# Performance work log

Hardware: AMD Instinct MI355X
Metric: run time of the kernel (lower is better)

Reference implementation:

```python
import jax, jax.numpy as jnp
import numpy as np

D_MODEL = 1024
HEADS = 16
D_K = D_MODEL // HEADS
D_FF = 4096
B, S = 4, 2048
EPS = 1e-5


def _layer_norm(x, gamma, beta):
    mu = jnp.mean(x, axis=-1, keepdims=True)
    var = jnp.mean(jnp.square(x - mu), axis=-1, keepdims=True)
    return (x - mu) * jax.lax.rsqrt(var + EPS) * gamma + beta


def setup_inputs() -> dict:
    key = jax.random.key(0)
    ks = jax.random.split(key, 16)
    s_in = 1.0 / np.sqrt(D_MODEL)
    s_ff = 1.0 / np.sqrt(D_FF)
    inp = {
        "x": jax.random.normal(ks[0], (B, S, D_MODEL), dtype=jnp.float32),
        "src_mask": jnp.ones((B, 1, 1, S), dtype=jnp.int32),
        "Wq": jax.random.uniform(ks[1], (D_MODEL, D_MODEL), jnp.float32, -s_in, s_in),
        "bq": jnp.zeros((D_MODEL,), jnp.float32),
        "Wk": jax.random.uniform(ks[2], (D_MODEL, D_MODEL), jnp.float32, -s_in, s_in),
        "bk": jnp.zeros((D_MODEL,), jnp.float32),
        "Wv": jax.random.uniform(ks[3], (D_MODEL, D_MODEL), jnp.float32, -s_in, s_in),
        "bv": jnp.zeros((D_MODEL,), jnp.float32),
        "Wo": jax.random.uniform(ks[4], (D_MODEL, D_MODEL), jnp.float32, -s_in, s_in),
        "bo": jnp.zeros((D_MODEL,), jnp.float32),
        "W1": jax.random.uniform(ks[5], (D_MODEL, D_FF), jnp.float32, -s_in, s_in),
        "b1": jnp.zeros((D_FF,), jnp.float32),
        "W2": jax.random.uniform(ks[6], (D_FF, D_MODEL), jnp.float32, -s_ff, s_ff),
        "b2": jnp.zeros((D_MODEL,), jnp.float32),
        "g1": jnp.ones((D_MODEL,), jnp.float32),
        "be1": jnp.zeros((D_MODEL,), jnp.float32),
        "g2": jnp.ones((D_MODEL,), jnp.float32),
        "be2": jnp.zeros((D_MODEL,), jnp.float32),
    }
    return inp


def reference(x, src_mask, Wq, bq, Wk, bk, Wv, bv, Wo, bo, W1, b1, W2, b2, g1, be1, g2, be2):
    Bn, L, _ = x.shape
    # Self-attention (dropout=0 / eval)
    q = (x @ Wq + bq).reshape(Bn, L, HEADS, D_K).transpose(0, 2, 1, 3)  # [B,H,L,dk]
    k = (x @ Wk + bk).reshape(Bn, L, HEADS, D_K).transpose(0, 2, 1, 3)
    v = (x @ Wv + bv).reshape(Bn, L, HEADS, D_K).transpose(0, 2, 1, 3)
    scores = jnp.einsum("bhqd,bhkd->bhqk", q, k) / np.sqrt(D_K).astype(np.float32)
    scores = jnp.where(src_mask == 0, -jnp.inf, scores)
    attn = jax.nn.softmax(scores, axis=-1)
    out = jnp.einsum("bhqk,bhkd->bhqd", attn, v)
    out = out.transpose(0, 2, 1, 3).reshape(Bn, L, D_MODEL)
    attn_out = out @ Wo + bo
    x = _layer_norm(x + attn_out, g1, be1)
    # FFN
    ffn = jax.nn.relu(x @ W1 + b1) @ W2 + b2
    x = _layer_norm(x + ffn, g2, be2)
    return x
```

## Files before the change

kernel.cpp:

```cpp
#include <hip/hip_runtime.h>
#include <hip/hip_bf16.h>
#include <cstdint>
#include <cstddef>

typedef __bf16 bf16;
typedef __bf16 bf16x8 __attribute__((ext_vector_type(8)));
typedef float  f32x4  __attribute__((ext_vector_type(4)));
typedef unsigned short u16x4 __attribute__((ext_vector_type(4)));
typedef uint32_t u32x4 __attribute__((ext_vector_type(4)));

static constexpr int D_MODEL = 1024;
static constexpr int HEADS   = 16;
static constexpr int D_KH    = 64;
static constexpr int D_FF    = 4096;
static constexpr int BATCH   = 4;
static constexpr int SEQ     = 2048;
static constexpr int MROWS   = BATCH * SEQ;
static constexpr float QSCALE = 0.18033688011f;

#define VMCNT(n) asm volatile("s_waitcnt vmcnt(" #n ")" ::: "memory")
#define LGKM0()                                            \
  do {                                                     \
    asm volatile("s_waitcnt lgkmcnt(0)" ::: "memory");     \
    __builtin_amdgcn_sched_barrier(0);                     \
  } while (0)

__device__ __forceinline__ unsigned short bfbits(float f) {
  return __builtin_bit_cast(unsigned short, (bf16)f);
}
__device__ __forceinline__ float bf2f(unsigned short u) {
  return __builtin_bit_cast(float, (uint32_t)u << 16);
}

__device__ __forceinline__ void gload_lds16(const void* g, void* l) {
  __builtin_amdgcn_global_load_lds(
      (__attribute__((address_space(1))) uint32_t*)(uintptr_t)g,
      (__attribute__((address_space(3))) uint32_t*)(uintptr_t)l, 16, 0, 0);
}

struct PrepArgs {
  const float* x; bf16* xb;
  const int* mask; uint32_t* flags;
  const float* w1; const float* w2; const float* wx[4];
  bf16* w1t; bf16* w2t; bf16* wxt[4];
};
__global__ void k_prep(PrepArgs p) {
  __shared__ float tile[64][65];
  const int t = blockIdx.x;
  if (t < 4096) {
    int i = (t * 256 + threadIdx.x) * 8;
    const float4* q = (const float4*)(p.x + i);
    float4 a = q[0], b = q[1];
    bf16x8 v;
    v[0] = (bf16)a.x; v[1] = (bf16)a.y; v[2] = (bf16)a.z; v[3] = (bf16)a.w;
    v[4] = (bf16)b.x; v[5] = (bf16)b.y; v[6] = (bf16)b.z; v[7] = (bf16)b.w;
    *(bf16x8*)(p.xb + i) = v;
    return;
  }
  if (t == 4096) {
    __shared__ uint32_t sb[4];
    int tid = threadIdx.x;
    if (tid < 4) sb[tid] = 0;
    __syncthreads();
    if (tid < 128) {
      int b = tid >> 5, tt = tid & 31;
      const int4* q = (const int4*)(p.mask + b * SEQ + tt * 64);
      int all = 1;
#pragma unroll
      for (int i = 0; i < 16; ++i) {
        int4 v = q[i];
        all &= v.x & v.y & v.z & v.w;
      }
      if (all) atomicOr(&sb[b], 1u << tt);
    }
    __syncthreads();
    if (tid < 4) p.flags[tid] = sb[tid];
    return;
  }
  int u = t - 4097;
  const float* W;
  bf16* Wt;
  int K, N, k0, n0;
  if (u < 1024) {
    W = p.w1; Wt = p.w1t; K = 1024; N = 4096;
    k0 = (u & 15) * 64; n0 = (u >> 4) * 64;
  } else if (u < 2048) {
    int v = u - 1024;
    W = p.w2; Wt = p.w2t; K = 4096; N = 1024;
    k0 = (v & 63) * 64; n0 = (v >> 6) * 64;
  } else {
    int v = u - 2048;
    int which = v >> 8, vv = v & 255;
    W = p.wx[which]; Wt = p.wxt[which]; K = 1024; N = 1024;
    k0 = (vv & 15) * 64; n0 = (vv >> 4) * 64;
  }
  int c = threadIdx.x & 63, r0 = threadIdx.x >> 6;
#pragma unroll
  for (int i = 0; i < 16; ++i) {
    int r = r0 + i * 4;
    tile[r][c] = W[(size_t)(k0 + r) * N + n0 + c];
  }
  __syncthreads();
#pragma unroll
  for (int i = 0; i < 16; ++i) {
    int r = r0 + i * 4;
    Wt[(size_t)(n0 + r) * K + k0 + c] = (bf16)tile[c][r];
  }
}

enum { EP_RELU = 0, EP_O16 = 1, EP_QKV = 2 };

template <int EPI, int NREP>
__global__ __launch_bounds__(512, 2) void k_gemm8(
    const bf16* __restrict__ A, const bf16* __restrict__ Bt,
    const float* __restrict__ bias, const float* __restrict__ bias2,
    const float* __restrict__ bias3,
    void* __restrict__ Cout, void* __restrict__ C2, void* __restrict__ C3,
    int N, int K) {
  extern __shared__ char smem[];
  constexpr int BN = NREP * 64;
  constexpr int HB = NREP / 2;
  const int tid = threadIdx.x;
  const int lane = tid & 63;
  const int wid = tid >> 6;
  const int wm = wid >> 2, wn = wid & 3;
  const int l15 = lane & 15, l4 = lane >> 4;
  const int bx = blockIdx.x, by = blockIdx.y;
  const int NI = K >> 7;

  const int c0 = tid, c1 = tid + 512;
  const bf16* baseA0 = A + (size_t)(bx * 256 + (c0 >> 3)) * K + ((c0 & 7) ^ ((c0 >> 3) & 7)) * 8;
  const bf16* baseA1 = A + (size_t)(bx * 256 + (c1 >> 3)) * K + ((c1 & 7) ^ ((c1 >> 3) & 7)) * 8;
  const bf16* baseB0 = Bt + (size_t)(by * BN + (c0 >> 3)) * K + ((c0 & 7) ^ ((c0 >> 3) & 7)) * 8;
  const bf16* baseB1 = Bt + (size_t)(by * BN + (c1 >> 3)) * K + ((c1 & 7) ^ ((c1 >> 3) & 7)) * 8;
  const size_t rowK128 = (size_t)128 * K;

  auto stA = [&](int h, int t, int buf) {
    gload_lds16(baseA0 + h * rowK128 + t * 64, smem + buf * 32768 + h * 16384 + c0 * 16);
    gload_lds16(baseA1 + h * rowK128 + t * 64, smem + buf * 32768 + h * 16384 + c1 * 16);
  };
  auto stB = [&](int h, int t, int buf) {
    gload_lds16(baseB0 + h * rowK128 + t * 64,
                smem + 65536 + buf * (HB * 16384) + h * 16384 + c0 * 16);
    gload_lds16(baseB1 + h * rowK128 + t * 64,
                smem + 65536 + buf * (HB * 16384) + h * 16384 + c1 * 16);
  };

  const int ch0 = (l4 ^ (l15 & 7)) * 16;
  const int ch1 = ((4 + l4) ^ (l15 & 7)) * 16;
  const int aoff = l15 * 128;
  int boffh[NREP];
#pragma unroll
  for (int n = 0; n < NREP; ++n) {
    int rB = wn * (NREP * 16) + n * 16 + l15;
    boffh[n] = (rB >> 7) * 16384 + (rB & 127) * 128;
  }

  f32x4 acc[8][NREP] = {};
  bf16x8 breg[NREP][2];

  stA(0, 0, 0); stA(1, 0, 0); stB(0, 0, 0);
  if constexpr (HB == 2) stB(1, 0, 0);
  stA(0, 1, 1); stA(1, 1, 1); stB(0, 1, 1);
  if constexpr (HB == 2) stB(1, 1, 1);

  for (int i = 0; i < NI; ++i) {
    const int t1 = 2 * i + 1, t2 = 2 * i + 2;
    const bool notfirst = (i > 0), notlast = (i + 1 < NI);
#pragma unroll
    for (int p = 0; p < 8; ++p) {
      const int q = p & 3;
      const char* Ab = smem + (p >> 2) * 32768 + wm * 16384;
      const char* Bb = smem + 65536 + (p >> 2) * (HB * 16384);
      if (p == 0) {
        if (notfirst) {
          stA(0, t1, 1);
          VMCNT(2);
        } else {
          if constexpr (HB == 2) VMCNT(8); else VMCNT(6);
        }
        __builtin_amdgcn_s_barrier();
      } else if (p == 4) {
        if (notlast) {
          stA(0, t2, 0);
          VMCNT(2);
        } else {
          VMCNT(0);
        }
        __builtin_amdgcn_s_barrier();
      }
      if (q == 0) {
#pragma unroll
        for (int n = 0; n < NREP; ++n) {
          breg[n][0] = *(const bf16x8*)(Bb + boffh[n] + ch0);
          breg[n][1] = *(const bf16x8*)(Bb + boffh[n] + ch1);
        }
      }
      bf16x8 a0k0 = *(const bf16x8*)(Ab + (2 * q + 0) * 2048 + aoff + ch0);
      bf16x8 a0k1 = *(const bf16x8*)(Ab + (2 * q + 0) * 2048 + aoff + ch1);
      bf16x8 a1k0 = *(const bf16x8*)(Ab + (2 * q + 1) * 2048 + aoff + ch0);
      bf16x8 a1k1 = *(const bf16x8*)(Ab + (2 * q + 1) * 2048 + aoff + ch1);
      if (p == 1) { if (notfirst) stA(1, t1, 1); }
      else if (p == 2) { if (notfirst) stB(0, t1, 1); }
      else if (p == 3) { if constexpr (HB == 2) { if (notfirst) stB(1, t1, 1); } }
      else if (p == 5) { if (notlast) stA(1, t2, 0); }
      else if (p == 6) { if (notlast) stB(0, t2, 0); }
      else if (p == 7) { if constexpr (HB == 2) { if (notlast) stB(1, t2, 0); } }
      if (p != 0 && p != 4) __builtin_amdgcn_s_barrier();
      LGKM0();
      __builtin_amdgcn_s_setprio(1);
#pragma unroll
      for (int n = 0; n < NREP; ++n) {
        acc[2 * q + 0][n] = __builtin_amdgcn_mfma_f32_16x16x32_bf16(a0k0, breg[n][0], acc[2 * q + 0][n], 0, 0, 0);
        acc[2 * q + 0][n] = __builtin_amdgcn_mfma_f32_16x16x32_bf16(a0k1, breg[n][1], acc[2 * q + 0][n], 0, 0, 0);
        acc[2 * q + 1][n] = __builtin_amdgcn_mfma_f32_16x16x32_bf16(a1k0, breg[n][0], acc[2 * q + 1][n], 0, 0, 0);
        acc[2 * q + 1][n] = __builtin_amdgcn_mfma_f32_16x16x32_bf16(a1k1, breg[n][1], acc[2 * q + 1][n], 0, 0, 0);
      }
      __builtin_amdgcn_s_setprio(0);
      __builtin_amdgcn_s_barrier();
    }
  }

  constexpr int BPM = 1024 / BN;
  float bia[NREP];
#pragma unroll
  for (int n = 0; n < NREP; ++n) {
    int colL = wn * (NREP * 16) + n * 16 + l15;
    if constexpr (EPI == EP_QKV) {
      const int g = by / BPM;
      const float* bp = (g == 0) ? bias : (g == 1 ? bias2 : bias3);
      bia[n] = bp[(by % BPM) * BN + colL];
    } else {
      bia[n] = bias[by * BN + colL];
    }
  }
#pragma unroll
  for (int mf = 0; mf < 8; ++mf) {
    int row0 = bx * 256 + wm * 128 + mf * 16 + l4 * 4;
#pragma unroll
    for (int n = 0; n < NREP; ++n) {
      int colL = wn * (NREP * 16) + n * 16 + l15;
      if constexpr (EPI == EP_QKV) {
        const int g = by / BPM;
        int cc = (by % BPM) * BN + colL;
        if (g == 2) {
          int bidx = row0 >> 11, s0 = row0 & 2047;
          u16x4 pk;
#pragma unroll
          for (int r = 0; r < 4; ++r) pk[r] = bfbits(acc[mf][n][r] + bia[n]);
          *(u16x4*)((bf16*)C3 + (((size_t)bidx * HEADS + (cc >> 6)) * D_KH + (cc & 63)) * SEQ + s0) = pk;
        } else if (g == 0) {
          bf16* dst = (bf16*)Cout;
#pragma unroll
          for (int r = 0; r < 4; ++r)
            dst[(size_t)(row0 + r) * 1024 + cc] = (bf16)((acc[mf][n][r] + bia[n]) * QSCALE);
        } else {
          bf16* dst = (bf16*)C2;
#pragma unroll
          for (int r = 0; r < 4; ++r)
            dst[(size_t)(row0 + r) * 1024 + cc] = (bf16)(acc[mf][n][r] + bia[n]);
        }
      } else {
        int col = by * BN + colL;
#pragma unroll
        for (int r = 0; r < 4; ++r) {
          float v = acc[mf][n][r] + bia[n];
          if constexpr (EPI == EP_RELU) v = fmaxf(v, 0.f);
          ((bf16*)Cout)[(size_t)(row0 + r) * N + col] = (bf16)v;
        }
      }
    }
  }
}

__global__ __launch_bounds__(256, 4) void k_attn(
    const bf16* __restrict__ Q, const bf16* __restrict__ Kb,
    const bf16* __restrict__ Vt, const int* __restrict__ mask,
    const uint32_t* __restrict__ Mf, bf16* __restrict__ O) {
  __shared__ bf16 Ks[2][64 * 64];
  __shared__ bf16 Vs[2][64 * 64];
  const int tid = threadIdx.x;
  const int lane = tid & 63;
  const int l15 = lane & 15, l4 = lane >> 4;
  const int L = blockIdx.x;
  const int xcd = L & 7, rest = L >> 3;
  const int qx = rest & 15, yhi = rest >> 4;
  const int bh = yhi * 8 + xcd;
  const int b = bh >> 4, h = bh & 15;
  const size_t qrow0 = (size_t)b * SEQ + qx * 128 + (tid >> 6) * 32;
  const bf16* Kbase = Kb + (size_t)b * SEQ * D_MODEL + h * 64;
  const bf16* Vbase = Vt + (size_t)bh * D_KH * SEQ;
  const int* mbase = mask + b * SEQ;
  const uint32_t mflags = Mf[b];

  bf16x8 qf[2][2];
#pragma unroll
  for (int m = 0; m < 2; ++m)
#pragma unroll
    for (int ks = 0; ks < 2; ++ks)
      qf[m][ks] = *(const bf16x8*)&Q[(qrow0 + m * 16 + l15) * D_MODEL + h * 64 + ks * 32 + l4 * 8];

  f32x4 o[2][4] = {};
  f32x4 rs[2] = {};
  bf16x8 ones;
#pragma unroll
  for (int i = 0; i < 8; ++i) ones[i] = (bf16)1.0f;

  const int koff0 = l15 * 64 + ((l4 * 8) ^ ((l15 & 7) << 3));
  const int koff1 = l15 * 64 + ((32 + l4 * 8) ^ ((l15 & 7) << 3));

  auto stage = [&](int buf, int kv0) {
#pragma unroll
    for (int i = 0; i < 2; ++i) {
      int o_ = tid + i * 256;
      int row = o_ >> 3;
      int ch = (o_ & 7) ^ (row & 7);
      gload_lds16(Kbase + (size_t)(kv0 + row) * D_MODEL + ch * 8,
                  (char*)&Ks[buf][0] + o_ * 16);
      gload_lds16(Vbase + (size_t)row * SEQ + kv0 + ch * 8,
                  (char*)&Vs[buf][0] + o_ * 16);
    }
  };

  stage(0, 0);
  __syncthreads();

  for (int kv0 = 0; kv0 < SEQ; kv0 += 64) {
    const int cur = (kv0 >> 6) & 1;
    if (kv0 + 64 < SEQ) stage(cur ^ 1, kv0 + 64);
    const bf16* Kc = &Ks[cur][0];
    const bf16* Vc = &Vs[cur][0];

    f32x4 sf[2][4] = {};
    __builtin_amdgcn_s_setprio(1);
#pragma unroll
    for (int ks = 0; ks < 2; ++ks)
#pragma unroll
      for (int n = 0; n < 4; ++n) {
        bf16x8 kf = *(const bf16x8*)&Kc[(ks ? koff1 : koff0) + n * 1024];
#pragma unroll
        for (int m = 0; m < 2; ++m)
          sf[m][n] = __builtin_amdgcn_mfma_f32_16x16x32_bf16(kf, qf[m][ks], sf[m][n], 0, 0, 0);
      }
    __builtin_amdgcn_s_setprio(0);

    if (__builtin_expect(!((mflags >> (kv0 >> 6)) & 1), 0)) {
#pragma unroll
      for (int n = 0; n < 4; ++n) {
        int4 mk = *(const int4*)&mbase[kv0 + n * 16 + l4 * 4];
#pragma unroll
        for (int r = 0; r < 4; ++r)
          if (((const int*)&mk)[r] == 0) {
            sf[0][n][r] = -1e30f;
            sf[1][n][r] = -1e30f;
          }
      }
    }

    uint32_t pk[2][4][2];
#pragma unroll
    for (int m = 0; m < 2; ++m) {
#pragma unroll
      for (int n = 0; n < 4; ++n) {
#pragma unroll
        for (int r = 0; r < 4; ++r) sf[m][n][r] = exp2f(sf[m][n][r]);
        asm("v_cvt_pk_bf16_f32 %0, %1, %2"
            : "=v"(pk[m][n][0]) : "v"(sf[m][n][0]), "v"(sf[m][n][1]));
        asm("v_cvt_pk_bf16_f32 %0, %1, %2"
            : "=v"(pk[m][n][1]) : "v"(sf[m][n][2]), "v"(sf[m][n][3]));
      }
    }

    bf16x8 pa[2][2];
#pragma unroll
    for (int m = 0; m < 2; ++m)
#pragma unroll
      for (int ks = 0; ks < 2; ++ks) {
        u32x4 w;
#pragma unroll
        for (int hh = 0; hh < 2; ++hh) {
          uint32_t a = pk[m][ks * 2 + 0][hh];
          uint32_t bsw = pk[m][ks * 2 + 1][hh];
          asm("v_permlane32_swap_b32 %0, %1" : "+v"(a), "+v"(bsw));
          asm("v_permlane16_swap_b32 %0, %1" : "+v"(a), "+v"(bsw));
          w[hh] = a;
          w[2 + hh] = bsw;
        }
        pa[ks][m] = __builtin_bit_cast(bf16x8, w);
      }

#pragma unroll
    for (int ks = 0; ks < 2; ++ks) {
      __builtin_amdgcn_s_setprio(1);
#pragma unroll
      for (int n = 0; n < 4; ++n) {
        bf16x8 vf = *(const bf16x8*)&Vc[(ks ? koff1 : koff0) + n * 1024];
#pragma unroll
        for (int m = 0; m < 2; ++m)
          o[m][n] = __builtin_amdgcn_mfma_f32_16x16x32_bf16(pa[ks][m], vf, o[m][n], 0, 0, 0);
      }
#pragma unroll
      for (int m = 0; m < 2; ++m)
        rs[m] = __builtin_amdgcn_mfma_f32_16x16x32_bf16(pa[ks][m], ones, rs[m], 0, 0, 0);
      __builtin_amdgcn_s_setprio(0);
    }
    __syncthreads();
  }

#pragma unroll
  for (int m = 0; m < 2; ++m) {
    float inv[4];
#pragma unroll
    for (int r = 0; r < 4; ++r) inv[r] = 1.0f / rs[m][r];
#pragma unroll
    for (int n = 0; n < 4; ++n)
#pragma unroll
      for (int r = 0; r < 4; ++r)
        O[(qrow0 + m * 16 + l4 * 4 + r) * D_MODEL + h * 64 + n * 16 + l15] =
            (bf16)(o[m][n][r] * inv[r]);
  }
}

__global__ __launch_bounds__(256) void k_add_ln1(
    const bf16* __restrict__ a, const bf16* __restrict__ b,
    const float* __restrict__ g, const float* __restrict__ be,
    bf16* __restrict__ y) {
  const int t = threadIdx.x;
  const size_t base = (size_t)blockIdx.x * D_MODEL + t * 4;
  u16x4 va = *(const u16x4*)(a + base);
  u16x4 vb = *(const u16x4*)(b + base);
  float v0 = bf2f(va[0]) + bf2f(vb[0]), v1 = bf2f(va[1]) + bf2f(vb[1]);
  float v2 = bf2f(va[2]) + bf2f(vb[2]), v3 = bf2f(va[3]) + bf2f(vb[3]);
  float s  = v0 + v1 + v2 + v3;
  float s2 = v0 * v0 + v1 * v1 + v2 * v2 + v3 * v3;
#pragma unroll
  for (int off = 1; off < 64; off <<= 1) {
    s  += __shfl_xor(s, off);
    s2 += __shfl_xor(s2, off);
  }
  __shared__ float red1[4], red2[4];
  int w = t >> 6;
  if ((t & 63) == 0) { red1[w] = s; red2[w] = s2; }
  __syncthreads();
  s  = red1[0] + red1[1] + red1[2] + red1[3];
  s2 = red2[0] + red2[1] + red2[2] + red2[3];
  float mu  = s * (1.f / D_MODEL);
  float var = s2 * (1.f / D_MODEL) - mu * mu;
  float rstd = rsqrtf(var + 1e-5f);
  float4 vg  = *(const float4*)(g + t * 4);
  float4 vbe = *(const float4*)(be + t * 4);
  u16x4 pk = {bfbits((v0 - mu) * rstd * vg.x + vbe.x),
              bfbits((v1 - mu) * rstd * vg.y + vbe.y),
              bfbits((v2 - mu) * rstd * vg.z + vbe.z),
              bfbits((v3 - mu) * rstd * vg.w + vbe.w)};
  *(u16x4*)(y + base) = pk;
}

__global__ __launch_bounds__(256) void k_add_ln2(
    const bf16* __restrict__ a, const bf16* __restrict__ b,
    const float* __restrict__ g, const float* __restrict__ be,
    float* __restrict__ y) {
  const int t = threadIdx.x;
  const size_t base = (size_t)blockIdx.x * D_MODEL + t * 4;
  u16x4 va = *(const u16x4*)(a + base);
  u16x4 vb = *(const u16x4*)(b + base);
  float v0 = bf2f(va[0]) + bf2f(vb[0]), v1 = bf2f(va[1]) + bf2f(vb[1]);
  float v2 = bf2f(va[2]) + bf2f(vb[2]), v3 = bf2f(va[3]) + bf2f(vb[3]);
  float s  = v0 + v1 + v2 + v3;
  float s2 = v0 * v0 + v1 * v1 + v2 * v2 + v3 * v3;
#pragma unroll
  for (int off = 1; off < 64; off <<= 1) {
    s  += __shfl_xor(s, off);
    s2 += __shfl_xor(s2, off);
  }
  __shared__ float red1[4], red2[4];
  int w = t >> 6;
  if ((t & 63) == 0) { red1[w] = s; red2[w] = s2; }
  __syncthreads();
  s  = red1[0] + red1[1] + red1[2] + red1[3];
  s2 = red2[0] + red2[1] + red2[2] + red2[3];
  float mu  = s * (1.f / D_MODEL);
  float var = s2 * (1.f / D_MODEL) - mu * mu;
  float rstd = rsqrtf(var + 1e-5f);
  float4 vg  = *(const float4*)(g + t * 4);
  float4 vbe = *(const float4*)(be + t * 4);
  *(float4*)(y + base) = make_float4((v0 - mu) * rstd * vg.x + vbe.x,
                                     (v1 - mu) * rstd * vg.y + vbe.y,
                                     (v2 - mu) * rstd * vg.z + vbe.z,
                                     (v3 - mu) * rstd * vg.w + vbe.w);
}

extern "C" void kernel_launch(void* const* d_in, const int* in_sizes, int n_in,
                              void* d_out, int out_size, void* d_ws, size_t ws_size,
                              hipStream_t stream) {
  const float* x   = (const float*)d_in[0];
  const int*  mask = (const int*)d_in[1];
  const float* Wq  = (const float*)d_in[2];
  const float* bq  = (const float*)d_in[3];
  const float* Wk  = (const float*)d_in[4];
  const float* bk_ = (const float*)d_in[5];
  const float* Wv  = (const float*)d_in[6];
  const float* bv  = (const float*)d_in[7];
  const float* Wo  = (const float*)d_in[8];
  const float* bo  = (const float*)d_in[9];
  const float* W1  = (const float*)d_in[10];
  const float* b1  = (const float*)d_in[11];
  const float* W2  = (const float*)d_in[12];
  const float* b2  = (const float*)d_in[13];
  const float* g1  = (const float*)d_in[14];
  const float* be1 = (const float*)d_in[15];
  const float* g2  = (const float*)d_in[16];
  const float* be2 = (const float*)d_in[17];

  char* ws = (char*)d_ws;
  const size_t MB = 1ull << 20;
  bf16*  xb    = (bf16*)(ws + 0);
  bf16*  Qb    = (bf16*)(ws + 16 * MB);
  bf16*  Kbuf  = (bf16*)(ws + 32 * MB);
  bf16*  Vt    = (bf16*)(ws + 48 * MB);
  bf16*  Hb    = (bf16*)(ws + 0);
  bf16*  aproj = (bf16*)(ws + 64 * MB);
  bf16*  f2o   = (bf16*)(ws + 80 * MB);
  bf16*  Ob    = (bf16*)(ws + 96 * MB);
  uint32_t* mfl = (uint32_t*)(ws + 112 * MB);
  bf16*  x1b   = (bf16*)(ws + 128 * MB);
  bf16*  Wqkvt = (bf16*)(ws + 144 * MB);
  bf16*  Wot   = (bf16*)(ws + 150 * MB);
  bf16*  W1t   = (bf16*)(ws + 152 * MB);
  bf16*  W2t   = (bf16*)(ws + 160 * MB);

  const int SM4 = 131072, SM2 = 98304;
  hipFuncSetAttribute(reinterpret_cast<const void*>(&k_gemm8<EP_QKV, 2>),
                      hipFuncAttributeMaxDynamicSharedMemorySize, SM2);
  hipFuncSetAttribute(reinterpret_cast<const void*>(&k_gemm8<EP_RELU, 4>),
                      hipFuncAttributeMaxDynamicSharedMemorySize, SM4);
  hipFuncSetAttribute(reinterpret_cast<const void*>(&k_gemm8<EP_O16, 2>),
                      hipFuncAttributeMaxDynamicSharedMemorySize, SM2);

  PrepArgs pp;
  pp.x = x; pp.xb = xb; pp.mask = mask; pp.flags = mfl;
  pp.w1 = W1; pp.w1t = W1t;
  pp.w2 = W2; pp.w2t = W2t;
  pp.wx[0] = Wq; pp.wxt[0] = Wqkvt;
  pp.wx[1] = Wk; pp.wxt[1] = Wqkvt + 1024 * 1024;
  pp.wx[2] = Wv; pp.wxt[2] = Wqkvt + 2 * 1024 * 1024;
  pp.wx[3] = Wo; pp.wxt[3] = Wot;
  k_prep<<<7169, 256, 0, stream>>>(pp);

  k_gemm8<EP_QKV, 2><<<dim3(32, 24), 512, SM2, stream>>>(
      xb, Wqkvt, bq, bk_, bv, Qb, Kbuf, Vt, 3072, 1024);

  k_attn<<<1024, 256, 0, stream>>>(Qb, Kbuf, Vt, mask, mfl, Ob);

  k_gemm8<EP_O16, 2><<<dim3(32, 8), 512, SM2, stream>>>(
      Ob, Wot, bo, nullptr, nullptr, aproj, nullptr, nullptr, 1024, 1024);
  k_add_ln1<<<MROWS, 256, 0, stream>>>(xb, aproj, g1, be1, x1b);

  k_gemm8<EP_RELU, 4><<<dim3(32, 16), 512, SM4, stream>>>(
      x1b, W1t, b1, nullptr, nullptr, Hb, nullptr, nullptr, 4096, 1024);
  k_gemm8<EP_O16, 2><<<dim3(32, 8), 512, SM2, stream>>>(
      Hb, W2t, b2, nullptr, nullptr, f2o, nullptr, nullptr, 1024, 4096);
  k_add_ln2<<<MROWS, 256, 0, stream>>>(x1b, f2o, g2, be2, (float*)d_out);
}
```

Measured before the change: 352.3 us.

## Transpose MFMA operands for vectorized GEMM epilogue stores; precompute attention staging pointers

For the non-QKV GEMM variants, the MFMA operands are swapped so each lane holds four consecutive output columns instead of four rows. This lets the bias be loaded as a float4 and the bf16 results written as one 8-byte packed store per fragment, replacing four scattered 2-byte stores. The attention kernel's K/V staging now precomputes global and LDS pointers once and advances them each tile, removing per-iteration index arithmetic. The operand swap changes the accumulator layout, so correctness depends on the new epilogue indexing matching the transposed fragments.

```diff
diff --git a/kernel.cpp b/kernel.cpp
--- a/kernel.cpp
+++ b/kernel.cpp
@@ -211,36 +211,39 @@
       __builtin_amdgcn_s_setprio(1);
 #pragma unroll
       for (int n = 0; n < NREP; ++n) {
-        acc[2 * q + 0][n] = __builtin_amdgcn_mfma_f32_16x16x32_bf16(a0k0, breg[n][0], acc[2 * q + 0][n], 0, 0, 0);
-        acc[2 * q + 0][n] = __builtin_amdgcn_mfma_f32_16x16x32_bf16(a0k1, breg[n][1], acc[2 * q + 0][n], 0, 0, 0);
-        acc[2 * q + 1][n] = __builtin_amdgcn_mfma_f32_16x16x32_bf16(a1k0, breg[n][0], acc[2 * q + 1][n], 0, 0, 0);
-        acc[2 * q + 1][n] = __builtin_amdgcn_mfma_f32_16x16x32_bf16(a1k1, breg[n][1], acc[2 * q + 1][n], 0, 0, 0);
+        if constexpr (EPI == EP_QKV) {
+          acc[2 * q + 0][n] = __builtin_amdgcn_mfma_f32_16x16x32_bf16(a0k0, breg[n][0], acc[2 * q + 0][n], 0, 0, 0);
+          acc[2 * q + 0][n] = __builtin_amdgcn_mfma_f32_16x16x32_bf16(a0k1, breg[n][1], acc[2 * q + 0][n], 0, 0, 0);
+          acc[2 * q + 1][n] = __builtin_amdgcn_mfma_f32_16x16x32_bf16(a1k0, breg[n][0], acc[2 * q + 1][n], 0, 0, 0);
+          acc[2 * q + 1][n] = __builtin_amdgcn_mfma_f32_16x16x32_bf16(a1k1, breg[n][1], acc[2 * q + 1][n], 0, 0, 0);
+        } else {
+          acc[2 * q + 0][n] = __builtin_amdgcn_mfma_f32_16x16x32_bf16(breg[n][0], a0k0, acc[2 * q + 0][n], 0, 0, 0);
+          acc[2 * q + 0][n] = __builtin_amdgcn_mfma_f32_16x16x32_bf16(breg[n][1], a0k1, acc[2 * q + 0][n], 0, 0, 0);
+          acc[2 * q + 1][n] = __builtin_amdgcn_mfma_f32_16x16x32_bf16(breg[n][0], a1k0, acc[2 * q + 1][n], 0, 0, 0);
+          acc[2 * q + 1][n] = __builtin_amdgcn_mfma_f32_16x16x32_bf16(breg[n][1], a1k1, acc[2 * q + 1][n], 0, 0, 0);
+        }
       }
       __builtin_amdgcn_s_setprio(0);
       __builtin_amdgcn_s_barrier();
     }
   }
 
-  constexpr int BPM = 1024 / BN;
-  float bia[NREP];
-#pragma unroll
-  for (int n = 0; n < NREP; ++n) {
-    int colL = wn * (NREP * 16) + n * 16 + l15;
-    if constexpr (EPI == EP_QKV) {
+  if constexpr (EPI == EP_QKV) {
+    constexpr int BPM = 1024 / BN;
+    float bia[NREP];
+#pragma unroll
+    for (int n = 0; n < NREP; ++n) {
+      int colL = wn * (NREP * 16) + n * 16 + l15;
       const int g = by / BPM;
       const float* bp = (g == 0) ? bias : (g == 1 ? bias2 : bias3);
       bia[n] = bp[(by % BPM) * BN + colL];
-    } else {
-      bia[n] = bias[by * BN + colL];
-    }
-  }
-#pragma unroll
-  for (int mf = 0; mf < 8; ++mf) {
-    int row0 = bx * 256 + wm * 128 + mf * 16 + l4 * 4;
-#pragma unroll
-    for (int n = 0; n < NREP; ++n) {
-      int colL = wn * (NREP * 16) + n * 16 + l15;
-      if constexpr (EPI == EP_QKV) {
+    }
+#pragma unroll
+    for (int mf = 0; mf < 8; ++mf) {
+      int row0 = bx * 256 + wm * 128 + mf * 16 + l4 * 4;
+#pragma unroll
+      for (int n = 0; n < NREP; ++n) {
+        int colL = wn * (NREP * 16) + n * 16 + l15;
         const int g = by / BPM;
         int cc = (by % BPM) * BN + colL;
         if (g == 2) {
@@ -260,14 +263,30 @@
           for (int r = 0; r < 4; ++r)
             dst[(size_t)(row0 + r) * 1024 + cc] = (bf16)(acc[mf][n][r] + bia[n]);
         }
-      } else {
-        int col = by * BN + colL;
-#pragma unroll
-        for (int r = 0; r < 4; ++r) {
-          float v = acc[mf][n][r] + bia[n];
-          if constexpr (EPI == EP_RELU) v = fmaxf(v, 0.f);
-          ((bf16*)Cout)[(size_t)(row0 + r) * N + col] = (bf16)v;
-        }
+      }
+    }
+  } else {
+    const int colbase = by * BN + wn * (NREP * 16);
+    float4 b4[NREP];
+#pragma unroll
+    for (int n = 0; n < NREP; ++n)
+      b4[n] = *(const float4*)&bias[colbase + n * 16 + l4 * 4];
+#pragma unroll
+    for (int mf = 0; mf < 8; ++mf) {
+      int row = bx * 256 + wm * 128 + mf * 16 + l15;
+      bf16* crow = (bf16*)Cout + (size_t)row * N + colbase;
+#pragma unroll
+      for (int n = 0; n < NREP; ++n) {
+        float v0 = acc[mf][n][0] + b4[n].x;
+        float v1 = acc[mf][n][1] + b4[n].y;
+        float v2 = acc[mf][n][2] + b4[n].z;
+        float v3 = acc[mf][n][3] + b4[n].w;
+        if constexpr (EPI == EP_RELU) {
+          v0 = fmaxf(v0, 0.f); v1 = fmaxf(v1, 0.f);
+          v2 = fmaxf(v2, 0.f); v3 = fmaxf(v3, 0.f);
+        }
+        u16x4 pk = {bfbits(v0), bfbits(v1), bfbits(v2), bfbits(v3)};
+        *(u16x4*)&crow[n * 16 + l4 * 4] = pk;
       }
     }
   }
@@ -309,25 +328,31 @@
   const int koff0 = l15 * 64 + ((l4 * 8) ^ ((l15 & 7) << 3));
   const int koff1 = l15 * 64 + ((32 + l4 * 8) ^ ((l15 & 7) << 3));
 
-  auto stage = [&](int buf, int kv0) {
-#pragma unroll
-    for (int i = 0; i < 2; ++i) {
-      int o_ = tid + i * 256;
-      int row = o_ >> 3;
-      int ch = (o_ & 7) ^ (row & 7);
-      gload_lds16(Kbase + (size_t)(kv0 + row) * D_MODEL + ch * 8,
-                  (char*)&Ks[buf][0] + o_ * 16);
-      gload_lds16(Vbase + (size_t)row * SEQ + kv0 + ch * 8,
-                  (char*)&Vs[buf][0] + o_ * 16);
-    }
+  const int r0_ = tid >> 3, c0_ = (tid & 7) ^ (r0_ & 7);
+  const int o1_ = tid + 256;
+  const int r1_ = o1_ >> 3, c1_ = (o1_ & 7) ^ (r1_ & 7);
+  const bf16* gK0 = Kbase + (size_t)r0_ * D_MODEL + c0_ * 8;
+  const bf16* gK1 = Kbase + (size_t)r1_ * D_MODEL + c1_ * 8;
+  const bf16* gV0 = Vbase + (size_t)r0_ * SEQ + c0_ * 8;
+  const bf16* gV1 = Vbase + (size_t)r1_ * SEQ + c1_ * 8;
+  char* ldsK = (char*)&Ks[0][0] + tid * 16;
+  char* ldsV = (char*)&Vs[0][0] + tid * 16;
+
+  auto stage = [&](int buf) {
+    gload_lds16(gK0, ldsK + buf * 8192);
+    gload_lds16(gK1, ldsK + buf * 8192 + 4096);
+    gload_lds16(gV0, ldsV + buf * 8192);
+    gload_lds16(gV1, ldsV + buf * 8192 + 4096);
+    gK0 += 64 * D_MODEL; gK1 += 64 * D_MODEL;
+    gV0 += 64; gV1 += 64;
   };
 
-  stage(0, 0);
+  stage(0);
   __syncthreads();
 
   for (int kv0 = 0; kv0 < SEQ; kv0 += 64) {
     const int cur = (kv0 >> 6) & 1;
-    if (kv0 + 64 < SEQ) stage(cur ^ 1, kv0 + 64);
+    if (kv0 + 64 < SEQ) stage(cur ^ 1);
     const bf16* Kc = &Ks[cur][0];
     const bf16* Vc = &Vs[cur][0];
 
```

New measurement: 359.9 us. +2.2%, slower.
